# Optimization experiments

Measured on AMD Instinct MI355X. Metric: run time of the kernel, lower is better.

Reference implementation:

```python
import jax, jax.numpy as jnp
import numpy as np

C, N = 3, 8192
FEATS = (64, 64, 1)
REG2, REG, REG_LENGTH = 1.0, 1.0, 4.0


def setup_inputs() -> dict:
    key = jax.random.key(0)
    k_x, k1, k2, k3 = jax.random.split(key, 4)
    x = jax.random.normal(k_x, (C, N), dtype=jnp.float32)
    # lecun_normal (flax Dense default): std = 1/sqrt(fan_in), no bias
    W1 = jax.random.normal(k1, (N, FEATS[0]), dtype=jnp.float32) / np.sqrt(N)
    W2 = jax.random.normal(k2, (FEATS[0], FEATS[1]), dtype=jnp.float32) / np.sqrt(FEATS[0])
    W3 = jax.random.normal(k3, (FEATS[1], FEATS[2]), dtype=jnp.float32) / np.sqrt(FEATS[1])
    regu2 = jnp.float32(REG2)
    regu = jnp.float32(REG)
    regu_length = jnp.float32(REG_LENGTH)
    return {"x": x, "W1": W1, "W2": W2, "W3": W3,
            "regu2": regu2, "regu": regu, "regu_length": regu_length}


def reference(x, W1, W2, W3, regu2, regu, regu_length):
    # x: (C, N)
    n = x.shape[1]
    # Circular cross-correlation rows: corr[i, j] = sum_c x[c, (i+j) % N] * x[c, i]
    corr = jax.vmap(
        lambda i: jnp.sum(jnp.roll(x, -i, axis=1) * x[:, i][:, None], axis=0)
    )(jnp.arange(n))  # (N, N)
    # tiny per-row MLP (Dense no-bias + elu), then sum over features
    z = jax.nn.elu(corr @ W1)
    z = jax.nn.elu(z @ W2)
    z = jax.nn.elu(z @ W3)
    per_row = jnp.sum(z, axis=-1)  # (N,)
    x2 = jnp.sum(x * x, axis=0)    # (N,)
    out = (jnp.mean(per_row)
           - regu2 * jnp.sum(x2)
           - regu * jnp.sum(jnp.exp(x2 / (2.0 * regu_length ** 2))))
    return out
```

## Files before the change

kernel.cpp:

```cpp
#include <hip/hip_runtime.h>
#include <hip/hip_bf16.h>

#define NN 8192
#define BM 32
#define BK 256
#define XD_LEN 16448
#define XW_LEN 304

typedef short bfrag8 __attribute__((ext_vector_type(8)));
typedef float floatx4 __attribute__((ext_vector_type(4)));

static __device__ __forceinline__ unsigned short f2bf(float f) {
  unsigned u = __builtin_bit_cast(unsigned, f);
  u = (u + 0x7FFFu + ((u >> 16) & 1u)) >> 16;
  return (unsigned short)u;
}
static __device__ __forceinline__ float bf2f(unsigned short h) {
  unsigned u = ((unsigned)h) << 16;
  return __builtin_bit_cast(float, u);
}
static __device__ __forceinline__ float elu(float v) {
  return v > 0.f ? v : expm1f(v);
}

__global__ void prep_kernel(const float* __restrict__ x, const float* __restrict__ W1,
                            const float* __restrict__ W2, const float* __restrict__ rlen,
                            unsigned short* __restrict__ W1T, unsigned short* __restrict__ W2T,
                            unsigned short* __restrict__ xd, float* __restrict__ acc) {
  const int b = blockIdx.x, t = threadIdx.x;
  if (b < 128) {
    __shared__ float tile[64][65];
    const int k0 = b * 64;
#pragma unroll
    for (int it = 0; it < 16; ++it) {
      int k = it * 4 + (t >> 6);
      tile[k][t & 63] = W1[(k0 + k) * 64 + (t & 63)];
    }
    __syncthreads();
#pragma unroll
    for (int it = 0; it < 16; ++it) {
      int f = it * 4 + (t >> 6);
      int kk = t & 63;
      W1T[f * NN + k0 + kk] = f2bf(tile[kk][f]);
    }
  } else if (b == 128) {
    for (int idx = t; idx < 64 * 64; idx += 256) {
      int k = idx >> 6, f = idx & 63;
      W2T[f * 64 + k] = f2bf(W2[idx]);
    }
  } else if (b == 129) {
    for (int c = 0; c < 3; ++c)
      for (int e = t * 4; e < XD_LEN; e += 1024) {
        float4 v = *(const float4*)&x[c * NN + (e & (NN - 1))];
        ushort4 o;
        o.x = f2bf(v.x); o.y = f2bf(v.y); o.z = f2bf(v.z); o.w = f2bf(v.w);
        *(ushort4*)&xd[c * XD_LEN + e] = o;
      }
  } else {
    float rl = rlen[0];
    float inv = 1.f / (2.f * rl * rl);
    int base = (b - 130) * 4096;
    float s1 = 0.f, s2 = 0.f;
    for (int ii = 0; ii < 16; ++ii) {
      int i = base + ii * 256 + t;
      float a0 = x[i], a1 = x[NN + i], a2 = x[2 * NN + i];
      float s = a0 * a0 + a1 * a1 + a2 * a2;
      s1 += s; s2 += expf(s * inv);
    }
    for (int d = 32; d > 0; d >>= 1) { s1 += __shfl_down(s1, d); s2 += __shfl_down(s2, d); }
    __shared__ float p1[4], p2[4];
    if ((t & 63) == 0) { p1[t >> 6] = s1; p2[t >> 6] = s2; }
    __syncthreads();
    if (t == 0) {
      atomicAdd(&acc[1], p1[0] + p1[1] + p1[2] + p1[3]);
      atomicAdd(&acc[2], p2[0] + p2[1] + p2[2] + p2[3]);
    }
  }
}

__global__ __launch_bounds__(512, 1) void main_kernel(
    const float* __restrict__ x, const unsigned short* __restrict__ W1T,
    const unsigned short* __restrict__ W2T, const unsigned short* __restrict__ xd,
    const float* __restrict__ W3, float* __restrict__ acc) {
  __shared__ __align__(16) unsigned short w1t[64 * 264];
  __shared__ __align__(16) unsigned short cr[BM * 264];
  __shared__ __align__(16) unsigned short xwin[2][3][XW_LEN];
  __shared__ float z3p[64];

  const int t = threadIdx.x;
  const int i0 = blockIdx.x * BM;
  const int w = t >> 6, l = t & 63;
  const int lg = l >> 4, lr = l & 15;

  const int cg = t & 31, rg = (t >> 5) & 7;
  const int r0 = rg * 4, jj0 = cg * 8;

  float xw[3][4];
  if (t < 256) {
#pragma unroll
    for (int c = 0; c < 3; ++c)
#pragma unroll
      for (int r = 0; r < 4; ++r)
        xw[c][r] = x[c * NN + i0 + r0 + r];
  }

  if (t < 114) {
    int c = t / 38, r = t - c * 38;
    *(uint4*)&xwin[0][c][r * 8] = *(const uint4*)&xd[c * XD_LEN + i0 + r * 8];
  }

  floatx4 acc00 = {0.f, 0.f, 0.f, 0.f}, acc01 = {0.f, 0.f, 0.f, 0.f};
  floatx4 acc10 = {0.f, 0.f, 0.f, 0.f}, acc11 = {0.f, 0.f, 0.f, 0.f};
  const int np = w & 1, quad = w >> 1;

  __syncthreads();

  for (int kt = 0; kt < NN / BK; ++kt) {
    const int j0 = kt * BK;
    const int buf = kt & 1;
    if (t < 256) {
      float accf[4][8];
#pragma unroll
      for (int r = 0; r < 4; ++r)
#pragma unroll
        for (int j = 0; j < 8; ++j) accf[r][j] = 0.f;
      const int s = r0 + jj0;
#pragma unroll
      for (int c = 0; c < 3; ++c) {
        const unsigned short* xb = &xwin[buf][c][s];
        ushort4 w0 = *(const ushort4*)(xb);
        ushort4 w1v = *(const ushort4*)(xb + 4);
        ushort4 w2v = *(const ushort4*)(xb + 8);
        float wf[12];
        wf[0] = bf2f(w0.x);  wf[1] = bf2f(w0.y);  wf[2] = bf2f(w0.z);  wf[3] = bf2f(w0.w);
        wf[4] = bf2f(w1v.x); wf[5] = bf2f(w1v.y); wf[6] = bf2f(w1v.z); wf[7] = bf2f(w1v.w);
        wf[8] = bf2f(w2v.x); wf[9] = bf2f(w2v.y); wf[10] = bf2f(w2v.z); wf[11] = bf2f(w2v.w);
#pragma unroll
        for (int r = 0; r < 4; ++r) {
          float wv = xw[c][r];
#pragma unroll
          for (int j = 0; j < 8; ++j) accf[r][j] = fmaf(wv, wf[r + j], accf[r][j]);
        }
      }
#pragma unroll
      for (int r = 0; r < 4; ++r) {
        unsigned q0 = (unsigned)f2bf(accf[r][0]) | ((unsigned)f2bf(accf[r][1]) << 16);
        unsigned q1 = (unsigned)f2bf(accf[r][2]) | ((unsigned)f2bf(accf[r][3]) << 16);
        unsigned q2 = (unsigned)f2bf(accf[r][4]) | ((unsigned)f2bf(accf[r][5]) << 16);
        unsigned q3 = (unsigned)f2bf(accf[r][6]) | ((unsigned)f2bf(accf[r][7]) << 16);
        uint4 q = {q0, q1, q2, q3};
        *(uint4*)&cr[(r0 + r) * 264 + jj0] = q;
      }
    } else {
      const int ts = t - 256;
      const int f = ts >> 2, qq = ts & 3;
      const int kp0 = qq * 64;
#pragma unroll
      for (int i = 0; i < 8; ++i) {
        *(uint4*)&w1t[f * 264 + kp0 + i * 8] =
            *(const uint4*)&W1T[f * NN + j0 + kp0 + i * 8];
      }
      if (kt + 1 < NN / BK && ts < 114) {
        int c = ts / 38, r = ts - c * 38;
        *(uint4*)&xwin[buf ^ 1][c][r * 8] =
            *(const uint4*)&xd[c * XD_LEN + i0 + j0 + BK + r * 8];
      }
    }
    __syncthreads();
#pragma unroll
    for (int s2 = 0; s2 < 2; ++s2) {
      const int kb = (quad + s2 * 4) * 32 + lg * 8;
      bfrag8 a0 = __builtin_bit_cast(bfrag8, *(const uint4*)&cr[lr * 264 + kb]);
      bfrag8 a1 = __builtin_bit_cast(bfrag8, *(const uint4*)&cr[(16 + lr) * 264 + kb]);
      bfrag8 b0 = __builtin_bit_cast(bfrag8, *(const uint4*)&w1t[(np * 32 + lr) * 264 + kb]);
      bfrag8 b1 = __builtin_bit_cast(bfrag8, *(const uint4*)&w1t[(np * 32 + 16 + lr) * 264 + kb]);
      acc00 = __builtin_amdgcn_mfma_f32_16x16x32_bf16(a0, b0, acc00, 0, 0, 0);
      acc01 = __builtin_amdgcn_mfma_f32_16x16x32_bf16(a0, b1, acc01, 0, 0, 0);
      acc10 = __builtin_amdgcn_mfma_f32_16x16x32_bf16(a1, b0, acc10, 0, 0, 0);
      acc11 = __builtin_amdgcn_mfma_f32_16x16x32_bf16(a1, b1, acc11, 0, 0, 0);
    }
    __syncthreads();
  }

  float* h1buf = (float*)cr;
  for (int q = t; q < 32 * 68; q += 512) h1buf[q] = 0.f;
  __syncthreads();
  {
#pragma unroll
    for (int m = 0; m < 2; ++m)
#pragma unroll
      for (int tn = 0; tn < 2; ++tn) {
        floatx4 a = (m == 0) ? (tn == 0 ? acc00 : acc01) : (tn == 0 ? acc10 : acc11);
#pragma unroll
        for (int r = 0; r < 4; ++r) {
          int row = m * 16 + lg * 4 + r;
          int col = np * 32 + tn * 16 + lr;
          atomicAdd(&h1buf[row * 68 + col], a[r]);
        }
      }
  }
  __syncthreads();

  if (t < 256) {
    const int m2 = w & 1, np2 = w >> 1;
    floatx4 acc2_0 = {0.f, 0.f, 0.f, 0.f}, acc2_1 = {0.f, 0.f, 0.f, 0.f};
#pragma unroll
    for (int ks2 = 0; ks2 < 2; ++ks2) {
      const int kb = ks2 * 32 + lg * 8;
      const float* hp = &h1buf[(m2 * 16 + lr) * 68 + kb];
      unsigned qa[4];
#pragma unroll
      for (int e = 0; e < 4; ++e) {
        float v0 = elu(hp[2 * e]), v1 = elu(hp[2 * e + 1]);
        qa[e] = (unsigned)f2bf(v0) | ((unsigned)f2bf(v1) << 16);
      }
      uint4 qv = {qa[0], qa[1], qa[2], qa[3]};
      bfrag8 a2 = __builtin_bit_cast(bfrag8, qv);
#pragma unroll
      for (int tn = 0; tn < 2; ++tn) {
        int col2 = np2 * 32 + tn * 16 + lr;
        bfrag8 b2 = __builtin_bit_cast(bfrag8, *(const uint4*)&W2T[col2 * 64 + kb]);
        if (tn == 0)
          acc2_0 = __builtin_amdgcn_mfma_f32_16x16x32_bf16(a2, b2, acc2_0, 0, 0, 0);
        else
          acc2_1 = __builtin_amdgcn_mfma_f32_16x16x32_bf16(a2, b2, acc2_1, 0, 0, 0);
      }
    }
    float w3a = W3[np2 * 32 + lr];
    float w3b = W3[np2 * 32 + 16 + lr];
    float vsum[4];
#pragma unroll
    for (int r = 0; r < 4; ++r) {
      float v = elu(acc2_0[r]) * w3a + elu(acc2_1[r]) * w3b;
      v += __shfl_xor(v, 1); v += __shfl_xor(v, 2);
      v += __shfl_xor(v, 4); v += __shfl_xor(v, 8);
      vsum[r] = v;
    }
    if (lr == 0) {
#pragma unroll
      for (int r = 0; r < 4; ++r)
        z3p[(m2 * 16 + lg * 4 + r) * 2 + np2] = vsum[r];
    }
  }
  __syncthreads();
  if (t < 32) {
    float sv = z3p[t * 2] + z3p[t * 2 + 1];
    float z3 = elu(sv);
    z3 += __shfl_xor(z3, 1); z3 += __shfl_xor(z3, 2); z3 += __shfl_xor(z3, 4);
    z3 += __shfl_xor(z3, 8); z3 += __shfl_xor(z3, 16);
    if (t == 0) atomicAdd(&acc[0], z3);
  }
}

__global__ void fin_kernel(const float* __restrict__ acc, const float* __restrict__ regu2,
                           const float* __restrict__ regu, float* __restrict__ out) {
  if (threadIdx.x == 0)
    out[0] = acc[0] * (1.f / (float)NN) - regu2[0] * acc[1] - regu[0] * acc[2];
}

extern "C" void kernel_launch(void* const* d_in, const int* in_sizes, int n_in,
                              void* d_out, int out_size, void* d_ws, size_t ws_size,
                              hipStream_t stream) {
  const float* x     = (const float*)d_in[0];
  const float* W1    = (const float*)d_in[1];
  const float* W2    = (const float*)d_in[2];
  const float* W3    = (const float*)d_in[3];
  const float* regu2 = (const float*)d_in[4];
  const float* regu  = (const float*)d_in[5];
  const float* rlen  = (const float*)d_in[6];

  char* ws = (char*)d_ws;
  float* acc            = (float*)ws;
  unsigned short* W1T   = (unsigned short*)(ws + 16);
  unsigned short* W2T   = (unsigned short*)(ws + 1048592);
  unsigned short* xd    = (unsigned short*)(ws + 1056784);

  (void)hipMemsetAsync(acc, 0, 16, stream);
  prep_kernel<<<132, 256, 0, stream>>>(x, W1, W2, rlen, W1T, W2T, xd, acc);
  main_kernel<<<256, 512, 0, stream>>>(x, W1T, W2T, xd, W3, acc);
  fin_kernel<<<1, 64, 0, stream>>>(acc, regu2, regu, (float*)d_out);
}
```

Baseline: 146.1 us.

## Load W1 fragments directly into registers and spread corr generation across all waves

The main loop is restructured. All 512 threads now compute the correlation tile; before, half the threads did that while the other half staged W1 through shared memory. B fragments are prefetched from global memory straight into registers one tile ahead. The correlation tile is double-buffered in a swizzled LDS layout, and a single barrier replaces two per iteration. The x window is kept in fp32 and staged from x directly, which drops the bf16 x copy and its prep block. This aims to cut LDS traffic and barriers and to overlap the global loads, at the cost of more register pressure and redundant W1 fragment loads per wave.

Result: faster. 120.3 us (-17.7%).

```diff
diff --git a/kernel.cpp b/kernel.cpp
--- a/kernel.cpp
+++ b/kernel.cpp
@@ -4,8 +4,8 @@
 #define NN 8192
 #define BM 32
 #define BK 256
-#define XD_LEN 16448
-#define XW_LEN 304
+#define NT (NN / BK)
+#define XWF 304
 
 typedef short bfrag8 __attribute__((ext_vector_type(8)));
 typedef float floatx4 __attribute__((ext_vector_type(4)));
@@ -15,9 +15,8 @@
   u = (u + 0x7FFFu + ((u >> 16) & 1u)) >> 16;
   return (unsigned short)u;
 }
-static __device__ __forceinline__ float bf2f(unsigned short h) {
-  unsigned u = ((unsigned)h) << 16;
-  return __builtin_bit_cast(float, u);
+static __device__ __forceinline__ unsigned cvt_pk_bf16(float a, float b) {
+  return (unsigned)f2bf(a) | ((unsigned)f2bf(b) << 16);
 }
 static __device__ __forceinline__ float elu(float v) {
   return v > 0.f ? v : expm1f(v);
@@ -26,7 +25,7 @@
 __global__ void prep_kernel(const float* __restrict__ x, const float* __restrict__ W1,
                             const float* __restrict__ W2, const float* __restrict__ rlen,
                             unsigned short* __restrict__ W1T, unsigned short* __restrict__ W2T,
-                            unsigned short* __restrict__ xd, float* __restrict__ acc) {
+                            float* __restrict__ acc) {
   const int b = blockIdx.x, t = threadIdx.x;
   if (b < 128) {
     __shared__ float tile[64][65];
@@ -48,18 +47,10 @@
       int k = idx >> 6, f = idx & 63;
       W2T[f * 64 + k] = f2bf(W2[idx]);
     }
-  } else if (b == 129) {
-    for (int c = 0; c < 3; ++c)
-      for (int e = t * 4; e < XD_LEN; e += 1024) {
-        float4 v = *(const float4*)&x[c * NN + (e & (NN - 1))];
-        ushort4 o;
-        o.x = f2bf(v.x); o.y = f2bf(v.y); o.z = f2bf(v.z); o.w = f2bf(v.w);
-        *(ushort4*)&xd[c * XD_LEN + e] = o;
-      }
   } else {
     float rl = rlen[0];
     float inv = 1.f / (2.f * rl * rl);
-    int base = (b - 130) * 4096;
+    int base = (b - 129) * 4096;
     float s1 = 0.f, s2 = 0.f;
     for (int ii = 0; ii < 16; ++ii) {
       int i = base + ii * 256 + t;
@@ -80,109 +71,118 @@
 
 __global__ __launch_bounds__(512, 1) void main_kernel(
     const float* __restrict__ x, const unsigned short* __restrict__ W1T,
-    const unsigned short* __restrict__ W2T, const unsigned short* __restrict__ xd,
-    const float* __restrict__ W3, float* __restrict__ acc) {
-  __shared__ __align__(16) unsigned short w1t[64 * 264];
-  __shared__ __align__(16) unsigned short cr[BM * 264];
-  __shared__ __align__(16) unsigned short xwin[2][3][XW_LEN];
+    const unsigned short* __restrict__ W2T, const float* __restrict__ W3,
+    float* __restrict__ acc) {
+  __shared__ __align__(16) unsigned short cr[2][BM * 256];
+  __shared__ __align__(16) float xwinf[2][3][XWF];
   __shared__ float z3p[64];
 
   const int t = threadIdx.x;
   const int i0 = blockIdx.x * BM;
-  const int w = t >> 6, l = t & 63;
+  const int wv = t >> 6;
+  const int l = t & 63;
   const int lg = l >> 4, lr = l & 15;
 
-  const int cg = t & 31, rg = (t >> 5) & 7;
-  const int r0 = rg * 4, jj0 = cg * 8;
-
-  float xw[3][4];
-  if (t < 256) {
-#pragma unroll
-    for (int c = 0; c < 3; ++c)
-#pragma unroll
-      for (int r = 0; r < 4; ++r)
-        xw[c][r] = x[c * NN + i0 + r0 + r];
-  }
-
-  if (t < 114) {
-    int c = t / 38, r = t - c * 38;
-    *(uint4*)&xwin[0][c][r * 8] = *(const uint4*)&xd[c * XD_LEN + i0 + r * 8];
-  }
+  const int cg = l;
+  const int sb = wv * 4 + cg * 4;
+
+  const int np = wv & 1, quad = wv >> 1;
+  const unsigned short* bp0 = W1T + (np * 32 + lr) * NN + quad * 32 + lg * 8;
+  const unsigned short* bp1 = bp0 + 16 * NN;
+
+  float xr[3][4];
+#pragma unroll
+  for (int c = 0; c < 3; ++c)
+#pragma unroll
+    for (int r = 0; r < 4; ++r)
+      xr[c][r] = x[c * NN + i0 + wv * 4 + r];
+
+  if (t < 216) {
+    int c = t / 72, rr = t - c * 72;
+    *(float4*)&xwinf[0][c][rr * 4] =
+        *(const float4*)&x[c * NN + ((i0 + rr * 4) & (NN - 1))];
+  }
+  uint4 bA0 = *(const uint4*)(bp0);
+  uint4 bA1 = *(const uint4*)(bp1);
+  uint4 bB0 = *(const uint4*)(bp0 + 128);
+  uint4 bB1 = *(const uint4*)(bp1 + 128);
 
   floatx4 acc00 = {0.f, 0.f, 0.f, 0.f}, acc01 = {0.f, 0.f, 0.f, 0.f};
   floatx4 acc10 = {0.f, 0.f, 0.f, 0.f}, acc11 = {0.f, 0.f, 0.f, 0.f};
-  const int np = w & 1, quad = w >> 1;
-
-  __syncthreads();
-
-  for (int kt = 0; kt < NN / BK; ++kt) {
+
+  __syncthreads();
+
+  for (int kt = 0; kt < NT; ++kt) {
     const int j0 = kt * BK;
     const int buf = kt & 1;
-    if (t < 256) {
-      float accf[4][8];
-#pragma unroll
-      for (int r = 0; r < 4; ++r)
-#pragma unroll
-        for (int j = 0; j < 8; ++j) accf[r][j] = 0.f;
-      const int s = r0 + jj0;
-#pragma unroll
-      for (int c = 0; c < 3; ++c) {
-        const unsigned short* xb = &xwin[buf][c][s];
-        ushort4 w0 = *(const ushort4*)(xb);
-        ushort4 w1v = *(const ushort4*)(xb + 4);
-        ushort4 w2v = *(const ushort4*)(xb + 8);
-        float wf[12];
-        wf[0] = bf2f(w0.x);  wf[1] = bf2f(w0.y);  wf[2] = bf2f(w0.z);  wf[3] = bf2f(w0.w);
-        wf[4] = bf2f(w1v.x); wf[5] = bf2f(w1v.y); wf[6] = bf2f(w1v.z); wf[7] = bf2f(w1v.w);
-        wf[8] = bf2f(w2v.x); wf[9] = bf2f(w2v.y); wf[10] = bf2f(w2v.z); wf[11] = bf2f(w2v.w);
-#pragma unroll
-        for (int r = 0; r < 4; ++r) {
-          float wv = xw[c][r];
-#pragma unroll
-          for (int j = 0; j < 8; ++j) accf[r][j] = fmaf(wv, wf[r + j], accf[r][j]);
-        }
-      }
+    const int jn = j0 + BK;
+    const bool more = (kt + 1 < NT);
+
+    float4 sv;
+    int c_st = 0, rr_st = 0;
+    const bool do_stage = more && (t < 216);
+    if (do_stage) {
+      c_st = t / 72; rr_st = t - c_st * 72;
+      sv = *(const float4*)&x[c_st * NN + ((i0 + jn + rr_st * 4) & (NN - 1))];
+    }
+    uint4 nA0, nA1, nB0, nB1;
+    if (more) {
+      nA0 = *(const uint4*)(bp0 + jn);
+      nA1 = *(const uint4*)(bp1 + jn);
+      nB0 = *(const uint4*)(bp0 + jn + 128);
+      nB1 = *(const uint4*)(bp1 + jn + 128);
+    }
+
+    float acf[4][4];
+#pragma unroll
+    for (int r = 0; r < 4; ++r)
+#pragma unroll
+      for (int j = 0; j < 4; ++j) acf[r][j] = 0.f;
+#pragma unroll
+    for (int c = 0; c < 3; ++c) {
+      const float* wp = &xwinf[buf][c][sb];
+      float4 v0 = *(const float4*)(wp);
+      float4 v1 = *(const float4*)(wp + 4);
+      float wf[7] = {v0.x, v0.y, v0.z, v0.w, v1.x, v1.y, v1.z};
 #pragma unroll
       for (int r = 0; r < 4; ++r) {
-        unsigned q0 = (unsigned)f2bf(accf[r][0]) | ((unsigned)f2bf(accf[r][1]) << 16);
-        unsigned q1 = (unsigned)f2bf(accf[r][2]) | ((unsigned)f2bf(accf[r][3]) << 16);
-        unsigned q2 = (unsigned)f2bf(accf[r][4]) | ((unsigned)f2bf(accf[r][5]) << 16);
-        unsigned q3 = (unsigned)f2bf(accf[r][6]) | ((unsigned)f2bf(accf[r][7]) << 16);
-        uint4 q = {q0, q1, q2, q3};
-        *(uint4*)&cr[(r0 + r) * 264 + jj0] = q;
-      }
-    } else {
-      const int ts = t - 256;
-      const int f = ts >> 2, qq = ts & 3;
-      const int kp0 = qq * 64;
-#pragma unroll
-      for (int i = 0; i < 8; ++i) {
-        *(uint4*)&w1t[f * 264 + kp0 + i * 8] =
-            *(const uint4*)&W1T[f * NN + j0 + kp0 + i * 8];
-      }
-      if (kt + 1 < NN / BK && ts < 114) {
-        int c = ts / 38, r = ts - c * 38;
-        *(uint4*)&xwin[buf ^ 1][c][r * 8] =
-            *(const uint4*)&xd[c * XD_LEN + i0 + j0 + BK + r * 8];
-      }
-    }
+        float xv = xr[c][r];
+#pragma unroll
+        for (int j = 0; j < 4; ++j) acf[r][j] = fmaf(xv, wf[r + j], acf[r][j]);
+      }
+    }
+#pragma unroll
+    for (int r = 0; r < 4; ++r) {
+      const int row = wv * 4 + r;
+      const int sw = ((cg >> 1) + 4 * row) & 31;
+      unsigned u0 = cvt_pk_bf16(acf[r][0], acf[r][1]);
+      unsigned u1 = cvt_pk_bf16(acf[r][2], acf[r][3]);
+      uint2 q = {u0, u1};
+      *(uint2*)((char*)&cr[buf][0] + row * 512 + sw * 16 + (cg & 1) * 8) = q;
+    }
+    if (do_stage) *(float4*)&xwinf[buf ^ 1][c_st][rr_st * 4] = sv;
+
     __syncthreads();
+
 #pragma unroll
     for (int s2 = 0; s2 < 2; ++s2) {
-      const int kb = (quad + s2 * 4) * 32 + lg * 8;
-      bfrag8 a0 = __builtin_bit_cast(bfrag8, *(const uint4*)&cr[lr * 264 + kb]);
-      bfrag8 a1 = __builtin_bit_cast(bfrag8, *(const uint4*)&cr[(16 + lr) * 264 + kb]);
-      bfrag8 b0 = __builtin_bit_cast(bfrag8, *(const uint4*)&w1t[(np * 32 + lr) * 264 + kb]);
-      bfrag8 b1 = __builtin_bit_cast(bfrag8, *(const uint4*)&w1t[(np * 32 + 16 + lr) * 264 + kb]);
+      const int slot = (quad + s2 * 4) * 4 + lg;
+      const int swz = (slot + 4 * lr) & 31;
+      bfrag8 a0 = __builtin_bit_cast(bfrag8,
+          *(const uint4*)((const char*)&cr[buf][0] + lr * 512 + swz * 16));
+      bfrag8 a1 = __builtin_bit_cast(bfrag8,
+          *(const uint4*)((const char*)&cr[buf][0] + (16 + lr) * 512 + swz * 16));
+      bfrag8 b0 = __builtin_bit_cast(bfrag8, s2 == 0 ? bA0 : bB0);
+      bfrag8 b1 = __builtin_bit_cast(bfrag8, s2 == 0 ? bA1 : bB1);
       acc00 = __builtin_amdgcn_mfma_f32_16x16x32_bf16(a0, b0, acc00, 0, 0, 0);
       acc01 = __builtin_amdgcn_mfma_f32_16x16x32_bf16(a0, b1, acc01, 0, 0, 0);
       acc10 = __builtin_amdgcn_mfma_f32_16x16x32_bf16(a1, b0, acc10, 0, 0, 0);
       acc11 = __builtin_amdgcn_mfma_f32_16x16x32_bf16(a1, b1, acc11, 0, 0, 0);
     }
-    __syncthreads();
-  }
-
-  float* h1buf = (float*)cr;
+    bA0 = nA0; bA1 = nA1; bB0 = nB0; bB1 = nB1;
+  }
+
+  float* h1buf = (float*)&cr[0][0];
   for (int q = t; q < 32 * 68; q += 512) h1buf[q] = 0.f;
   __syncthreads();
   {
@@ -202,7 +202,8 @@
   __syncthreads();
 
   if (t < 256) {
-    const int m2 = w & 1, np2 = w >> 1;
+    const int w4 = t >> 6;
+    const int m2 = w4 & 1, np2 = w4 >> 1;
     floatx4 acc2_0 = {0.f, 0.f, 0.f, 0.f}, acc2_1 = {0.f, 0.f, 0.f, 0.f};
 #pragma unroll
     for (int ks2 = 0; ks2 < 2; ++ks2) {
@@ -212,7 +213,7 @@
 #pragma unroll
       for (int e = 0; e < 4; ++e) {
         float v0 = elu(hp[2 * e]), v1 = elu(hp[2 * e + 1]);
-        qa[e] = (unsigned)f2bf(v0) | ((unsigned)f2bf(v1) << 16);
+        qa[e] = cvt_pk_bf16(v0, v1);
       }
       uint4 qv = {qa[0], qa[1], qa[2], qa[3]};
       bfrag8 a2 = __builtin_bit_cast(bfrag8, qv);
@@ -244,8 +245,8 @@
   }
   __syncthreads();
   if (t < 32) {
-    float sv = z3p[t * 2] + z3p[t * 2 + 1];
-    float z3 = elu(sv);
+    float sv2 = z3p[t * 2] + z3p[t * 2 + 1];
+    float z3 = elu(sv2);
     z3 += __shfl_xor(z3, 1); z3 += __shfl_xor(z3, 2); z3 += __shfl_xor(z3, 4);
     z3 += __shfl_xor(z3, 8); z3 += __shfl_xor(z3, 16);
     if (t == 0) atomicAdd(&acc[0], z3);
@@ -273,10 +274,9 @@
   float* acc            = (float*)ws;
   unsigned short* W1T   = (unsigned short*)(ws + 16);
   unsigned short* W2T   = (unsigned short*)(ws + 1048592);
-  unsigned short* xd    = (unsigned short*)(ws + 1056784);
 
   (void)hipMemsetAsync(acc, 0, 16, stream);
-  prep_kernel<<<132, 256, 0, stream>>>(x, W1, W2, rlen, W1T, W2T, xd, acc);
-  main_kernel<<<256, 512, 0, stream>>>(x, W1T, W2T, xd, W3, acc);
+  prep_kernel<<<131, 256, 0, stream>>>(x, W1, W2, rlen, W1T, W2T, acc);
+  main_kernel<<<256, 512, 0, stream>>>(x, W1T, W2T, W3, acc);
   fin_kernel<<<1, 64, 0, stream>>>(acc, regu2, regu, (float*)d_out);
 }
```
